# Kernel optimization log

Hardware: AMD Instinct MI355X
Metric: run time of the kernel (lower is better)

The kernel has to match this reference:

```python
import jax, jax.numpy as jnp
import numpy as np

B, S, E, H, L, D = 16, 512, 512, 8, 3, 64
OBS, ACT, NA = 128, 16, 8
KAPPAS = jnp.asarray(1.0 - 2.0 ** (-5.0 - np.arange(H)), jnp.float32)  # per-head retention decay, decay_scaling_factor=1.0
INV_SQRT_D = 1.0 / float(np.sqrt(D))


def rmsnorm(x, w, eps=1e-6):
    return x * jax.lax.rsqrt(jnp.mean(x * x, -1, keepdims=True) + eps) * w


def swiglu(x, wg, wp):
    return jax.nn.silu(x @ wg) * (x @ wp)


def sin_pe(ts, dim):
    # sinusoidal timestep positional encoding, ts: (B,S) float -> (B,S,dim)
    half = dim // 2
    freqs = jnp.exp(-np.log(10000.0) * jnp.arange(half, dtype=jnp.float32) / half)
    ang = ts[..., None] * freqs
    return jnp.concatenate([jnp.sin(ang), jnp.cos(ang)], -1)


def retention(xk, xq, xv, h0, ts, wq, wk, wv, wo, masked):
    # chunkwise multi-scale retention with cross-chunk recurrent state h0: (B,H,D,D)
    b, s, e = xq.shape
    pe = sin_pe(ts, e)
    q = ((xq + pe) @ wq).reshape(b, s, H, D).transpose(0, 2, 1, 3)            # (B,H,S,D)
    k = ((xk + pe) @ wk).reshape(b, s, H, D).transpose(0, 2, 1, 3) * INV_SQRT_D
    v = ((xv + pe) @ wv).reshape(b, s, H, D).transpose(0, 2, 1, 3)
    lk = jnp.log(KAPPAS)                                                      # (H,)
    diff = ts[:, None, :, None] - ts[:, None, None, :]                        # (B,1,S,S) timestep gaps
    if masked:
        idx = jnp.arange(s)
        allow = (diff > 0) | ((diff == 0) & (idx[:, None] >= idx[None, :]))
        dmat = jnp.where(allow, jnp.exp(lk[None, :, None, None] * diff), 0.0)
    else:
        dmat = jnp.exp(lk[None, :, None, None] * jnp.abs(diff))
    scores = jnp.einsum('bhnd,bhmd->bhnm', q, k) * dmat                       # decay-masked scores
    xi = jnp.exp(lk[None, :, None] * (ts[:, None, :] + 1.0))                  # (B,H,S) cross-chunk decay
    out = jnp.einsum('bhnm,bhmd->bhnd', scores, v) + jnp.einsum('bhnd,bhde->bhne', q, h0) * xi[..., None]
    tmax = ts.max(-1)                                                         # (B,)
    wst = jnp.exp(lk[None, :, None] * (tmax[:, None, None] - ts[:, None, :]))  # (B,H,S)
    h_new = jnp.exp(lk[None, :] * (tmax[:, None] + 1.0))[..., None, None] * h0 \
        + jnp.einsum('bhm,bhmd,bhme->bhde', wst, k, v)
    out = out.transpose(0, 2, 1, 3).reshape(b, s, e) @ wo
    return out, h_new


def _forward(obs, action, enc_hs, dec_hs1, dec_hs2, step_count, params):
    (eoln, eow, eln, ewq, ewk, ewv, ewo, eln1, eln2, efg, efp,
     ehw1, ehb1, ehln, ehw2, ehb2,
     daw, dln, dwq1, dwk1, dwv1, dwo1, dwq2, dwk2, dwv2, dwo2,
     dln1, dln2, dln3, dfg, dfp,
     dhw1, dhb1, dhln, dhw2, dhb2) = params
    ts = step_count.astype(jnp.float32)
    # ---- Encoder ----
    obs_rep = jax.nn.gelu(rmsnorm(obs, eoln) @ eow)
    enc_new = []
    for i in range(L):
        x = rmsnorm(obs_rep, eln)
        ret, hn = retention(x, x, x, enc_hs[:, i], ts, ewq[i], ewk[i], ewv[i], ewo[i], masked=False)
        x = rmsnorm(x + ret, eln1[i])
        obs_rep = rmsnorm(x + swiglu(x, efg[i], efp[i]), eln2[i])
        enc_new.append(hn)
    value = rmsnorm(jax.nn.gelu(obs_rep @ ehw1 + ehb1), ehln) @ ehw2 + ehb2
    # ---- Decoder ----
    x = rmsnorm(jax.nn.gelu(action @ daw), dln)
    d1_new, d2_new = [], []
    for i in range(L):
        ret, h1 = retention(x, x, x, dec_hs1[:, i], ts, dwq1[i], dwk1[i], dwv1[i], dwo1[i], masked=True)
        r = rmsnorm(x + ret, dln1[i])
        ret2, h2 = retention(r, obs_rep, r, dec_hs2[:, i], ts, dwq2[i], dwk2[i], dwv2[i], dwo2[i], masked=True)
        y = rmsnorm(obs_rep + ret2, dln2[i])
        x = rmsnorm(y + swiglu(y, dfg[i], dfp[i]), dln3[i])
        d1_new.append(h1)
        d2_new.append(h2)
    logits = rmsnorm(jax.nn.gelu(x @ dhw1 + dhb1), dhln) @ dhw2 + dhb2
    return value, logits, jnp.stack(enc_new, 1), jnp.stack(d1_new, 1), jnp.stack(d2_new, 1)


def setup_inputs():
    key = jax.random.key(0)
    ki = iter(jax.random.split(key, 50))
    def w(shape, s=0.02):
        return jax.random.normal(next(ki), shape, jnp.float32) * s
    inp = {
        'obs': jax.random.normal(next(ki), (B, S, OBS), jnp.float32),
        'action': jax.random.uniform(next(ki), (B, S, ACT + 1), jnp.float32),
        'enc_hs': jnp.zeros((B, L, H, D, D), jnp.float32),
        'dec_hs1': jnp.zeros((B, L, H, D, D), jnp.float32),
        'dec_hs2': jnp.zeros((B, L, H, D, D), jnp.float32),
        'step_count': jnp.broadcast_to(jnp.arange(S, dtype=jnp.int32) // NA, (B, S)),
        'enc_obs_ln_w': jnp.ones((OBS,), jnp.float32),
        'enc_obs_w': w((OBS, E)),
        'enc_ln_w': jnp.ones((E,), jnp.float32),
        'enc_wq': w((L, E, E)), 'enc_wk': w((L, E, E)), 'enc_wv': w((L, E, E)), 'enc_wo': w((L, E, E)),
        'enc_ln1_w': jnp.ones((L, E), jnp.float32), 'enc_ln2_w': jnp.ones((L, E), jnp.float32),
        'enc_ffn_gate': w((L, E, E)), 'enc_ffn_proj': w((L, E, E)),
        'enc_head_w1': w((E, E)), 'enc_head_b1': jnp.zeros((E,), jnp.float32),
        'enc_head_ln': jnp.ones((E,), jnp.float32),
        'enc_head_w2': w((E, 1)), 'enc_head_b2': jnp.zeros((1,), jnp.float32),
        'dec_act_w': w((ACT + 1, E)), 'dec_ln_w': jnp.ones((E,), jnp.float32),
        'dec_wq1': w((L, E, E)), 'dec_wk1': w((L, E, E)), 'dec_wv1': w((L, E, E)), 'dec_wo1': w((L, E, E)),
        'dec_wq2': w((L, E, E)), 'dec_wk2': w((L, E, E)), 'dec_wv2': w((L, E, E)), 'dec_wo2': w((L, E, E)),
        'dec_ln1_w': jnp.ones((L, E), jnp.float32), 'dec_ln2_w': jnp.ones((L, E), jnp.float32),
        'dec_ln3_w': jnp.ones((L, E), jnp.float32),
        'dec_ffn_gate': w((L, E, E)), 'dec_ffn_proj': w((L, E, E)),
        'dec_head_w1': w((E, E)), 'dec_head_b1': jnp.zeros((E,), jnp.float32),
        'dec_head_ln': jnp.ones((E,), jnp.float32),
        'dec_head_w2': w((E, ACT)), 'dec_head_b2': jnp.zeros((ACT,), jnp.float32),
    }
    return inp


def reference(obs, action, enc_hs, dec_hs1, dec_hs2, step_count, enc_obs_ln_w, enc_obs_w, enc_ln_w, enc_wq, enc_wk, enc_wv, enc_wo, enc_ln1_w, enc_ln2_w, enc_ffn_gate, enc_ffn_proj, enc_head_w1, enc_head_b1, enc_head_ln, enc_head_w2, enc_head_b2, dec_act_w, dec_ln_w, dec_wq1, dec_wk1, dec_wv1, dec_wo1, dec_wq2, dec_wk2, dec_wv2, dec_wo2, dec_ln1_w, dec_ln2_w, dec_ln3_w, dec_ffn_gate, dec_ffn_proj, dec_head_w1, dec_head_b1, dec_head_ln, dec_head_w2, dec_head_b2):
    params = (enc_obs_ln_w, enc_obs_w, enc_ln_w, enc_wq, enc_wk, enc_wv, enc_wo, enc_ln1_w, enc_ln2_w, enc_ffn_gate, enc_ffn_proj, enc_head_w1, enc_head_b1, enc_head_ln, enc_head_w2, enc_head_b2, dec_act_w, dec_ln_w, dec_wq1, dec_wk1, dec_wv1, dec_wo1, dec_wq2, dec_wk2, dec_wv2, dec_wo2, dec_ln1_w, dec_ln2_w, dec_ln3_w, dec_ffn_gate, dec_ffn_proj, dec_head_w1, dec_head_b1, dec_head_ln, dec_head_w2, dec_head_b2)
    return _forward(obs, action, enc_hs, dec_hs1, dec_hs2, step_count, params)
```

## Files before the change

kernel.cpp:

```cpp
#include <hip/hip_runtime.h>
#include <hip/hip_bf16.h>
#include <math.h>

typedef __attribute__((ext_vector_type(8))) short short8;
typedef __attribute__((ext_vector_type(4))) short short4v;
typedef __attribute__((ext_vector_type(4))) float f32x4;

#define BB 16
#define SS 512
#define EE 512
#define HH 8
#define DH 64
#define LL 3
#define MM (BB*SS)
#define OBSD 128
#define ACTD 17
#define INV_SQRT_D 0.125f

#define ACT_NONE 0
#define ACT_GELU 1

#define NORM_PLAIN 0
#define NORM_ADD 1

// ... 32 lines not shown
  for (int i = 0; i < 4; ++i){
    int k = gx*32 + ty + i*8, n = gy*32 + tx;
    t[ty+i*8][tx] = (k < K) ? src[(size_t)k*EE + n] : 0.f;
  }
  __syncthreads();
  #pragma unroll
  for (int i = 0; i < 4; ++i){
    int k = gx*32 + tx, n = gy*32 + ty + i*8;
    dst[(size_t)n*Kpad + k] = f2bs(t[tx][ty+i*8]);
  }
}

struct TP50 { const float* s[50]; unsigned short* d[50]; };
__global__ __launch_bounds__(256) void wtpose_batch_kernel(TP50 tp)
{
  __shared__ float t[32][33];
  const float* src = tp.s[blockIdx.z];
  unsigned short* dst = tp.d[blockIdx.z];
  const int gx = blockIdx.x, gy = blockIdx.y;
  const int tx = threadIdx.x, ty = threadIdx.y;
  #pragma unroll
  for (int i = 0; i < 4; ++i){
    int k = gx*32 + ty + i*8, n = gy*32 + tx;
    t[ty+i*8][tx] = src[(size_t)k*EE + n];
  }
  __syncthreads();
  #pragma unroll
  for (int i = 0; i < 4; ++i){
    int k = gx*32 + tx, n = gy*32 + ty + i*8;
    dst[(size_t)n*EE + k] = f2bs(t[tx][ty+i*8]);
  }
}

template<int MODE, int ENC>
__global__ __launch_bounds__(256) void gemm128_kernel(
    const unsigned short* __restrict__ A, const unsigned short* __restrict__ Wt,
    const float* __restrict__ bias, float* __restrict__ C,
    int Kpad, float scale, int act,
    int gstart, const int* __restrict__ tsi,
    unsigned short* __restrict__ qlo, unsigned short* __restrict__ qhi,
    unsigned short* __restrict__ klo, unsigned short* __restrict__ kloT,
    unsigned short* __restrict__ khi, unsigned short* __restrict__ khiT,
    unsigned short* __restrict__ vT)
{
  __shared__ unsigned short As[2][128*64];
  __shared__ unsigned short Bs[2][128*64];
  const int bm = blockIdx.y*128, bn = blockIdx.x*128;
  const int tid = threadIdx.x, lane = tid & 63, wv = tid >> 6;
  const int wr = wv >> 1, wc = wv & 1;
  const int l16 = lane & 15, quad = lane >> 4;

  f32x4 acc[4][4];
  #pragma unroll
  for (int i=0;i<4;i++)
    #pragma unroll
    for (int j=0;j<4;j++) acc[i][j]=(f32x4)(0.f);

  const int sg = lane >> 3;
  const int lg = (lane & 7) ^ sg;
  size_t aoff[4], boff[4];
  #pragma unroll
  for (int i=0;i<4;i++){
    aoff[i] = (size_t)(bm + wv*32 + i*8 + sg)*Kpad + lg*8;
    boff[i] = (size_t)(bn + wv*32 + i*8 + sg)*Kpad + lg*8;
  }
  const int swz = (l16 & 7) << 3;

  auto STAGE = [&](int buf, int t){
    const int k0 = t*64;
    #pragma unroll
    for (int i=0;i<4;i++){
      gl16(A + aoff[i] + k0, (char*)&As[buf][0] + ((wv*4+i) << 10));
      gl16(Wt + boff[i] + k0, (char*)&Bs[buf][0] + ((wv*4+i) << 10));
    }
  };
// ... 11 lines not shown
        bf[nt][ks] = *(const short8*)&Bs[buf][(wc*64 + nt*16 + l16)*64 + ((ks*32 + quad*8) ^ swz)];
    #pragma unroll
    for (int ks=0; ks<2; ++ks)
      #pragma unroll
      for (int mt=0; mt<4; ++mt)
        #pragma unroll
        for (int nt=0; nt<4; ++nt)
          acc[mt][nt] = __builtin_amdgcn_mfma_f32_16x16x32_bf16(af[mt][ks], bf[nt][ks], acc[mt][nt], 0, 0, 0);
  };

  const int NT = Kpad >> 6;
  STAGE(0, 0);
  PIPE_SYNC;
  int cur = 0;
  for (int t = 0; t < NT; ++t){
    if (t+1 < NT) STAGE(cur^1, t+1);
    COMPUTE(cur);
    if (t+1 < NT) PIPE_SYNC;
    cur ^= 1;
  }

  if (MODE == 0){
    #pragma unroll
    for (int mt=0; mt<4; ++mt){
      int rb = bm + wr*64 + mt*16 + quad*4;
      #pragma unroll
      for (int nt=0; nt<4; ++nt){
        int col = bn + wc*64 + nt*16 + l16;
        float bv = bias ? bias[col] : 0.f;
        #pragma unroll
        for (int j=0;j<4;j++){
          float v = acc[mt][nt][j]*scale + bv;
          if (act==ACT_GELU) v = gelu_f(v);
          C[(size_t)(rb+j)*EE + col] = v;
        }
      }
    }
  } else {
    const int group = gstart + (bn >> 9);
    const int hh = ((bn & 511) >> 6) + wc;
    const float lkh = lkappa(hh);
    const float scl = (group == 1) ? INV_SQRT_D : 1.f;
    const float dsg = (group == 1) ? -1.f : 1.f;
    #pragma unroll
    for (int mt=0; mt<4; ++mt){
      int rb = bm + wr*64 + mt*16 + quad*4;
      float e0[4], e1[4];
      if (group < 2){
        #pragma unroll
        for (int j=0;j<4;j++){
          float x = dsg*lkh*(float)tsi[rb+j];
          e0[j] = __expf(x); e1[j] = __expf(-x);
        }
      }
      int bloc = rb >> 9, m0 = rb & 511;
      #pragma unroll
      for (int nt=0; nt<4; ++nt){
        int ccol = (bn & 511) + wc*64 + nt*16 + l16;
        int ee = nt*16 + l16;
        size_t taddr = (((size_t)bloc*HH + hh)*DH + ee)*SS + m0;
        float vals[4];
        #pragma unroll
        for (int j=0;j<4;j++) vals[j] = acc[mt][nt][j]*scl;
        if (group == 0){
          #pragma unroll
          for (int j=0;j<4;j++) qlo[(size_t)(rb+j)*EE + ccol] = f2bs(vals[j]*e0[j]);
          if (ENC){
            #pragma unroll
            for (int j=0;j<4;j++) qhi[(size_t)(rb+j)*EE + ccol] = f2bs(vals[j]*e1[j]);
          }
        } else if (group == 1){
          short4v pk;
          #pragma unroll
          for (int j=0;j<4;j++){
            unsigned short v = f2bs(vals[j]*e0[j]);
            klo[(size_t)(rb+j)*EE + ccol] = v;
            pk[j] = (short)v;
          }
          *(short4v*)&kloT[taddr] = pk;
          if (ENC){
            short4v pk2;
            #pragma unroll
            for (int j=0;j<4;j++){
              unsigned short v = f2bs(vals[j]*e1[j]);
              khi[(size_t)(rb+j)*EE + ccol] = v;
              pk2[j] = (short)v;
            }
            *(short4v*)&khiT[taddr] = pk2;
          }
        } else {
          short4v pk;
          #pragma unroll
          for (int j=0;j<4;j++) pk[j] = (short)f2bs(vals[j]);
          *(short4v*)&vT[taddr] = pk;
        }
      }
    }
  }
}

__global__ __launch_bounds__(256) void gemm_sw_kernel(
    const unsigned short* __restrict__ A, const unsigned short* __restrict__ Wt,
    const unsigned short* __restrict__ Wt2, unsigned short* __restrict__ swo)
{
  __shared__ unsigned short As[2][128*64];
  __shared__ unsigned short Bs[2][64*64];
  __shared__ unsigned short Bs2[2][64*64];
  const int bm = blockIdx.y*128, bn = blockIdx.x*64;
  const int tid = threadIdx.x, lane = tid & 63, wv = tid >> 6;
  const int wr = wv >> 1, wc = wv & 1;
  const int l16 = lane & 15, quad = lane >> 4;

  f32x4 acc[4][2], acc2[4][2];
  #pragma unroll
  for (int i=0;i<4;i++){
    acc[i][0]=(f32x4)(0.f); acc[i][1]=(f32x4)(0.f);
    acc2[i][0]=(f32x4)(0.f); acc2[i][1]=(f32x4)(0.f);
  }

  const int sg = lane >> 3;
  const int lg = (lane & 7) ^ sg;
  size_t aoff[4], boff[2];
  #pragma unroll
  for (int i=0;i<4;i++)
    aoff[i] = (size_t)(bm + (wv*4+i)*8 + sg)*EE + lg*8;
  #pragma unroll
// ... 32 lines not shown
      #pragma unroll
      for (int mt=0; mt<4; ++mt)
        #pragma unroll
        for (int nt=0; nt<2; ++nt){
          acc[mt][nt]  = __builtin_amdgcn_mfma_f32_16x16x32_bf16(af[mt][ks], bf[nt][ks],  acc[mt][nt],  0, 0, 0);
          acc2[mt][nt] = __builtin_amdgcn_mfma_f32_16x16x32_bf16(af[mt][ks], bf2[nt][ks], acc2[mt][nt], 0, 0, 0);
        }
  };

  STAGE(0, 0);
  PIPE_SYNC;
  int cur = 0;
  for (int t = 0; t < 8; ++t){
    if (t+1 < 8) STAGE(cur^1, t+1);
    COMPUTE(cur);
    if (t+1 < 8) PIPE_SYNC;
    cur ^= 1;
  }

  #pragma unroll
  for (int mt=0; mt<4; ++mt){
    int rb = bm + wr*64 + mt*16 + quad*4;
    #pragma unroll
    for (int nt=0; nt<2; ++nt){
      int col = bn + wc*32 + nt*16 + l16;
      #pragma unroll
      for (int j=0;j<4;j++)
        swo[(size_t)(rb+j)*EE + col] = f2bs(silu_f(acc[mt][nt][j])*acc2[mt][nt][j]);
    }
  }
}

__global__ __launch_bounds__(256) void norm_b_kernel(
    const float* __restrict__ af, const unsigned short* __restrict__ ab,
    const float* __restrict__ res, const unsigned short* __restrict__ resb,
    const float* __restrict__ w, unsigned short* __restrict__ o1,
    unsigned short* __restrict__ o2, const unsigned short* __restrict__ peb,
    int mode)
{
  const int row = blockIdx.x*4 + (threadIdx.x >> 6);
  const int lane = threadIdx.x & 63;
  const size_t base = (size_t)row*EE + lane*8;
  float t[8];
  if (ab){
    short8 av = *(const short8*)&ab[base];
    #pragma unroll
    for (int e=0;e<8;++e) t[e] = bs2f((unsigned short)av[e]);
  } else {
    float4 a0 = *(const float4*)&af[base];
    float4 a1 = *(const float4*)&af[base+4];
    t[0]=a0.x;t[1]=a0.y;t[2]=a0.z;t[3]=a0.w;t[4]=a1.x;t[5]=a1.y;t[6]=a1.z;t[7]=a1.w;
  }
  if (mode == NORM_ADD){
    if (resb){
      short8 rv = *(const short8*)&resb[base];
      #pragma unroll
      for (int e=0;e<8;++e) t[e] += bs2f((unsigned short)rv[e]);
    } else {
      float4 r0 = *(const float4*)&res[base];
      float4 r1 = *(const float4*)&res[base+4];
      t[0]+=r0.x;t[1]+=r0.y;t[2]+=r0.z;t[3]+=r0.w;t[4]+=r1.x;t[5]+=r1.y;t[6]+=r1.z;t[7]+=r1.w;
    }
  }
  float ss = 0.f;
  #pragma unroll
  for (int e=0;e<8;++e) ss += t[e]*t[e];
  #pragma unroll
  for (int o=32;o;o>>=1) ss += __shfl_xor(ss, o);
  float r = 1.f/sqrtf(ss/(float)EE + 1e-6f);
  float4 w0 = *(const float4*)&w[lane*8];
  float4 w1 = *(const float4*)&w[lane*8+4];
  float y[8];
  y[0]=t[0]*r*w0.x; y[1]=t[1]*r*w0.y; y[2]=t[2]*r*w0.z; y[3]=t[3]*r*w0.w;
  y[4]=t[4]*r*w1.x; y[5]=t[5]*r*w1.y; y[6]=t[6]*r*w1.z; y[7]=t[7]*r*w1.w;
  short8 pk;
  #pragma unroll
  for (int e=0;e<8;++e) pk[e] = (short)f2bs(y[e]);
  *(short8*)&o1[base] = pk;
  if (o2){
    short8 pv = *(const short8*)&peb[base];
    short8 pz;
    #pragma unroll
    for (int e=0;e<8;++e) pz[e] = (short)f2bs(y[e] + bs2f((unsigned short)pv[e]));
    *(short8*)&o2[base] = pz;
  }
}

__global__ __launch_bounds__(256) void norm_obs_kernel(
    const float* __restrict__ a, const float* __restrict__ w, unsigned short* __restrict__ o)
{
  const int row = blockIdx.x*4 + (threadIdx.x >> 6);
  const int lane = threadIdx.x & 63;
  const size_t base = (size_t)row*OBSD + lane*2;
  float2 av = *(const float2*)&a[base];
  float ss = av.x*av.x + av.y*av.y;
  #pragma unroll
  for (int off=32;off;off>>=1) ss += __shfl_xor(ss, off);
  float r = 1.f/sqrtf(ss/(float)OBSD + 1e-6f);
  float2 wv2 = *(const float2*)&w[lane*2];
  unsigned int pk = (unsigned int)f2bs(av.x*r*wv2.x) | ((unsigned int)f2bs(av.y*r*wv2.y) << 16);
  *(unsigned int*)&o[base] = pk;
}

__global__ __launch_bounds__(256) void act_embed_kernel(
    const float* __restrict__ a, unsigned short* __restrict__ o)
{
  int idx = blockIdx.x*256 + threadIdx.x;
  int row = idx >> 6, col = idx & 63;
  o[idx] = (col < ACTD) ? f2bs(a[(size_t)row*ACTD + col]) : 0;
}

__global__ __launch_bounds__(256) void wchunkscan_kernel(
    const unsigned short* __restrict__ kloT, const unsigned short* __restrict__ khiT,
    const unsigned short* __restrict__ vT,
    const float* __restrict__ h0, const float* __restrict__ tmx,
    unsigned short* __restrict__ wcum_lo, unsigned short* __restrict__ wcum_hi,
    float* __restrict__ hnew, int enc)
{
  __shared__ unsigned short vsh[64*72];
  __shared__ unsigned short ksh[64*72];
  const int h = blockIdx.x, b = blockIdx.y;
  const int tid = threadIdx.x, lane = tid & 63, wv = tid >> 6;
  const int quad = lane >> 4, l16 = lane & 15;
  const float lk = lkappa(h);
  const float elk = __expf(lk);
  const float etm = __expf(lk*tmx[b]);
  const size_t wbase = ((size_t)b*HH + h)*8*4096;
  const size_t hbase = (size_t)b*(LL*HH*DH*DH) + (size_t)h*(DH*DH);
  const int e0r = wv*16 + quad*4;
  const int sr = tid >> 2, sseg = (tid & 3)*16;

  f32x4 cum[4];
  #pragma unroll
  for (int dt=0; dt<4; ++dt)
    #pragma unroll
    for (int j=0;j<4;j++)
      cum[dt][j] = elk * h0[hbase + (size_t)(dt*16+l16)*64 + e0r + j];

  for (int c = 0; c < 8; ++c){
    __syncthreads();
    {
      const unsigned short* vrow = vT   + (((size_t)b*HH + h)*DH + sr)*SS + c*64 + sseg;
      const unsigned short* krow = kloT + (((size_t)b*HH + h)*DH + sr)*SS + c*64 + sseg;
      #pragma unroll
      for (int i = 0; i < 2; ++i){
        *(short8*)&vsh[sr*72 + sseg + i*8] = *(const short8*)(vrow + i*8);
        *(short8*)&ksh[sr*72 + sseg + i*8] = *(const short8*)(krow + i*8);
      }
    }
    __syncthreads();
    short8 av[2];
    #pragma unroll
    for (int ks=0; ks<2; ++ks)
      av[ks] = *(const short8*)&vsh[(wv*16 + l16)*72 + ks*32 + quad*8];
    f32x4 acc[4];
    #pragma unroll
    for (int dt=0; dt<4; ++dt) acc[dt] = (f32x4)(0.f);
    #pragma unroll
    for (int ks=0; ks<2; ++ks)
      #pragma unroll
      for (int dt=0; dt<4; ++dt){
        short8 kb = *(const short8*)&ksh[(dt*16 + l16)*72 + ks*32 + quad*8];
        acc[dt] = __builtin_amdgcn_mfma_f32_16x16x32_bf16(av[ks], kb, acc[dt], 0, 0, 0);
      }
    #pragma unroll
    for (int dt=0; dt<4; ++dt)
      #pragma unroll
      for (int j=0;j<4;j++){
        wcum_lo[wbase + (size_t)c*4096 + (size_t)(e0r+j)*64 + dt*16 + l16] = f2bs(cum[dt][j]);
        cum[dt][j] += acc[dt][j];
      }
  }
  #pragma unroll
  for (int dt=0; dt<4; ++dt)
    #pragma unroll
    for (int j=0;j<4;j++)
      hnew[hbase + (size_t)(dt*16+l16)*64 + e0r + j] = etm * cum[dt][j];

  if (enc){
    f32x4 suf[4];
    #pragma unroll
    for (int dt=0; dt<4; ++dt) suf[dt] = (f32x4)(0.f);
    for (int c = 7; c >= 0; --c){
      __syncthreads();
      {
        const unsigned short* vrow = vT   + (((size_t)b*HH + h)*DH + sr)*SS + c*64 + sseg;
        const unsigned short* krow = khiT + (((size_t)b*HH + h)*DH + sr)*SS + c*64 + sseg;
        #pragma unroll
        for (int i = 0; i < 2; ++i){
          *(short8*)&vsh[sr*72 + sseg + i*8] = *(const short8*)(vrow + i*8);
          *(short8*)&ksh[sr*72 + sseg + i*8] = *(const short8*)(krow + i*8);
        }
      }
      __syncthreads();
      short8 av[2];
      #pragma unroll
      for (int ks=0; ks<2; ++ks)
        av[ks] = *(const short8*)&vsh[(wv*16 + l16)*72 + ks*32 + quad*8];
      f32x4 acc[4];
      #pragma unroll
      for (int dt=0; dt<4; ++dt) acc[dt] = (f32x4)(0.f);
      #pragma unroll
      for (int ks=0; ks<2; ++ks)
        #pragma unroll
        for (int dt=0; dt<4; ++dt){
          short8 kb = *(const short8*)&ksh[(dt*16 + l16)*72 + ks*32 + quad*8];
          acc[dt] = __builtin_amdgcn_mfma_f32_16x16x32_bf16(av[ks], kb, acc[dt], 0, 0, 0);
        }
      #pragma unroll
      for (int dt=0; dt<4; ++dt)
        #pragma unroll
        for (int j=0;j<4;j++){
          wcum_hi[wbase + (size_t)c*4096 + (size_t)(e0r+j)*64 + dt*16 + l16] = f2bs(suf[dt][j]);
          suf[dt][j] += acc[dt][j];
        }
    }
  }
}

template<int ENC>
__global__ __launch_bounds__(256) void retention2_kernel(
    const unsigned short* __restrict__ qlo, const unsigned short* __restrict__ qhi,
    const unsigned short* __restrict__ klo, const unsigned short* __restrict__ khi,
    const unsigned short* __restrict__ vT,
    const unsigned short* __restrict__ wlo, const unsigned short* __restrict__ whi,
    const int* __restrict__ tsi, unsigned short* __restrict__ outp)
{
  __shared__ unsigned short qsh[64*72];
  __shared__ unsigned short wsh[64*72];
  __shared__ unsigned short ksh[64*72];
  __shared__ unsigned short vsh[64*72];
  __shared__ unsigned short qsh2[ENC ? 64*72 : 2];
  __shared__ unsigned short wsh2[ENC ? 64*72 : 2];
  __shared__ float tsf[SS];
  const int b = blockIdx.z, h = blockIdx.y, t = blockIdx.x;
  const int n0 = t*64;
  const int tid = threadIdx.x, lane = tid & 63, wv = tid >> 6;
  const int quad = lane >> 4, l16 = lane & 15;

  for (int i = tid; i < SS; i += 256) tsf[i] = (float)tsi[b*SS + i];
  {
    const int n = tid >> 2, seg = (tid & 3)*16;
    const unsigned short* qr = qlo + ((size_t)b*SS + n0 + n)*EE + h*DH + seg;
    #pragma unroll
    for (int i = 0; i < 2; ++i)
      *(short8*)&qsh[n*72 + seg + i*8] = *(const short8*)(qr + i*8);
    const unsigned short* wr = wlo + (((size_t)b*HH + h)*8 + t)*4096 + (size_t)n*64 + seg;
    #pragma unroll
    for (int i = 0; i < 2; ++i)
      *(short8*)&wsh[n*72 + seg + i*8] = *(const short8*)(wr + i*8);
    if (ENC){
      const unsigned short* qr2 = qhi + ((size_t)b*SS + n0 + n)*EE + h*DH + seg;
      #pragma unroll
      for (int i = 0; i < 2; ++i)
        *(short8*)&qsh2[n*72 + seg + i*8] = *(const short8*)(qr2 + i*8);
      const unsigned short* wr2 = whi + (((size_t)b*HH + h)*8 + t)*4096 + (size_t)n*64 + seg;
      #pragma unroll
      for (int i = 0; i < 2; ++i)
        *(short8*)&wsh2[n*72 + seg + i*8] = *(const short8*)(wr2 + i*8);
    }
  }
  __syncthreads();

  const int rowbase = wv*16;
  short8 qa[2], qa2[2];
  #pragma unroll
  for (int ks=0; ks<2; ++ks)
    qa[ks] = *(const short8*)&qsh[(rowbase + l16)*72 + ks*32 + quad*8];
  if (ENC){
    #pragma unroll
    for (int ks=0; ks<2; ++ks)
      qa2[ks] = *(const short8*)&qsh2[(rowbase + l16)*72 + ks*32 + quad*8];
  }

  float tn = tsf[n0 + lane];
  float maxn = tn, minn = tn;
  #pragma unroll
  for (int o=32;o;o>>=1){
    maxn = fmaxf(maxn, __shfl_xor(maxn, o));
    minn = fminf(minn, __shfl_xor(minn, o));
  }

  f32x4 acc_o[4];
  #pragma unroll
  for (int et=0; et<4; ++et){
    f32x4 a = (f32x4)(0.f);
    #pragma unroll
    for (int ks=0; ks<2; ++ks){
      short8 wb = *(const short8*)&wsh[(et*16 + l16)*72 + ks*32 + quad*8];
      a = __builtin_amdgcn_mfma_f32_16x16x32_bf16(qa[ks], wb, a, 0, 0, 0);
    }
    if (ENC){
      #pragma unroll
      for (int ks=0; ks<2; ++ks){
        short8 wb2 = *(const short8*)&wsh2[(et*16 + l16)*72 + ks*32 + quad*8];
        a = __builtin_amdgcn_mfma_f32_16x16x32_bf16(qa2[ks], wb2, a, 0, 0, 0);
      }
    }
    acc_o[et] = a;
  }

  for (int c = 0; c < 8; ++c){
    const int mc = c*64;
    float tmv = tsf[mc + lane];
    float maxm = tmv, minm = tmv;
    #pragma unroll
    for (int o=32;o;o>>=1){
      maxm = fmaxf(maxm, __shfl_xor(maxm, o));
      minm = fminf(minm, __shfl_xor(minm, o));
    }
    if (ENC){
      if (maxm <= minn) continue;
      if (minm >= maxn) continue;
    } else {
      if ((maxm < minn) || (maxm == minn && (mc + 63) < n0)) continue;
      if (minm > maxn) continue;
    }
    __syncthreads();
    {
      const int m = tid >> 2, cb = (tid & 3)*16;
      const unsigned short* krow = klo + ((size_t)b*SS + mc + m)*EE + h*DH + cb;
      #pragma unroll
      for (int i = 0; i < 2; ++i)
        *(short8*)&ksh[m*72 + cb + i*8] = *(const short8*)(krow + i*8);
      const unsigned short* vrow = vT + (((size_t)b*HH + h)*DH + m)*SS + mc + cb;
      #pragma unroll
      for (int i = 0; i < 2; ++i)
        *(short8*)&vsh[m*72 + cb + i*8] = *(const short8*)(vrow + i*8);
      if (ENC){
        const unsigned short* k2row = khi + ((size_t)b*SS + mc + m)*EE + h*DH + cb;
        #pragma unroll
        for (int i = 0; i < 2; ++i)
          *(short8*)&qsh2[m*72 + cb + i*8] = *(const short8*)(k2row + i*8);
      }
    }
    __syncthreads();
    f32x4 sacc[4], sacc2[4];
    #pragma unroll
    for (int mt=0; mt<4; ++mt){
      f32x4 a = (f32x4)(0.f);
      #pragma unroll
      for (int ks=0; ks<2; ++ks){
        short8 kb = *(const short8*)&ksh[(mt*16 + l16)*72 + ks*32 + quad*8];
        a = __builtin_amdgcn_mfma_f32_16x16x32_bf16(qa[ks], kb, a, 0, 0, 0);
      }
      sacc[mt] = a;
      if (ENC){
        f32x4 a2 = (f32x4)(0.f);
        #pragma unroll
        for (int ks=0; ks<2; ++ks){
          short8 kb2 = *(const short8*)&qsh2[(mt*16 + l16)*72 + ks*32 + quad*8];
          a2 = __builtin_amdgcn_mfma_f32_16x16x32_bf16(qa2[ks], kb2, a2, 0, 0, 0);
        }
        sacc2[mt] = a2;
      }
    }
    float tsm[4]; int mg[4];
    #pragma unroll
    for (int mt=0; mt<4; ++mt){ mg[mt] = mc + mt*16 + l16; tsm[mt] = tsf[mg[mt]]; }
    #pragma unroll
    for (int j=0;j<4;j++){
      int nloc = rowbase + quad*4 + j;
      int n = n0 + nloc;
      float tsn = tsf[n];
      #pragma unroll
      for (int mt=0; mt<4; ++mt){
        float diff = tsn - tsm[mt];
// ... 120 lines not shown
  const float* ehw1 = (const float*)d_in[17];
  const float* ehb1 = (const float*)d_in[18];
  const float* ehln = (const float*)d_in[19];
  const float* ehw2 = (const float*)d_in[20];
  const float* ehb2 = (const float*)d_in[21];
  const float* daw  = (const float*)d_in[22];
  const float* dln  = (const float*)d_in[23];
  const float* dwq1 = (const float*)d_in[24];
  const float* dwk1 = (const float*)d_in[25];
  const float* dwv1 = (const float*)d_in[26];
  const float* dwo1 = (const float*)d_in[27];
  const float* dwq2 = (const float*)d_in[28];
  const float* dwk2 = (const float*)d_in[29];
  const float* dwv2 = (const float*)d_in[30];
  const float* dwo2 = (const float*)d_in[31];
  const float* dln1 = (const float*)d_in[32];
  const float* dln2 = (const float*)d_in[33];
  const float* dln3 = (const float*)d_in[34];
  const float* dfg  = (const float*)d_in[35];
  const float* dfp  = (const float*)d_in[36];
  const float* dhw1 = (const float*)d_in[37];
  const float* dhb1 = (const float*)d_in[38];
  const float* dhln = (const float*)d_in[39];
  const float* dhw2 = (const float*)d_in[40];
  const float* dhb2 = (const float*)d_in[41];

  const size_t BUF = (size_t)MM*EE;
  float* wsf  = (float*)d_ws;
  float* f32a = wsf;
  float* f32b = f32a + BUF;
  float* tmx  = f32b + BUF;
  unsigned short* wcum_lo = (unsigned short*)f32a;
  unsigned short* wcum_hi = wcum_lo + BUF;
  unsigned short* sw_b    = (unsigned short*)f32b;
  unsigned short* ub = (unsigned short*)(tmx + 64);
  unsigned short* xrep_b    = ub;  ub += BUF;
  unsigned short* xrep_pe_b = ub;  ub += BUF;
  unsigned short* x_b       = ub;  ub += BUF;
  unsigned short* x_pe_b    = ub;  ub += BUF;
  unsigned short* t1_b      = ub;  ub += BUF;
  unsigned short* t1_pe_b   = ub;  ub += BUF;
  unsigned short* peb       = ub;  ub += BUF;
  unsigned short* qlo_b     = ub;  ub += BUF;
  unsigned short* klo_b     = ub;  ub += BUF;
  unsigned short* kloT_b    = ub;  ub += BUF;
  unsigned short* khi_b     = ub;  ub += BUF;
  unsigned short* khiT_b    = ub;  ub += BUF;
  unsigned short* vT_b      = ub;  ub += BUF;
  unsigned short* obs_n     = ub;  ub += (size_t)MM*OBSD;
  unsigned short* act_b     = obs_n;
  unsigned short* qhi_b     = t1_pe_b;
  const size_t W55 = (size_t)EE*EE;
  unsigned short* wts = ub;  ub += 50*W55;
  unsigned short* wt_eow = ub; ub += (size_t)EE*OBSD;
  unsigned short* wt_daw = ub; ub += (size_t)EE*64;
  size_t need = (char*)ub - (char*)d_ws;
  if (ws_size < need) return;

  unsigned short* wt_eqkv  = wts + 0*W55;
  unsigned short* wt_ewo   = wts + 9*W55;
  unsigned short* wt_efg   = wts + 12*W55;
  unsigned short* wt_efp   = wts + 15*W55;
  unsigned short* wt_ehw1  = wts + 18*W55;
  unsigned short* wt_dqkv1 = wts + 19*W55;
  unsigned short* wt_dwo1  = wts + 28*W55;
  unsigned short* wt_dkv2  = wts + 31*W55;
  unsigned short* wt_dwq2  = wts + 37*W55;
  unsigned short* wt_dwo2  = wts + 40*W55;
  unsigned short* wt_dfg   = wts + 43*W55;
  unsigned short* wt_dfp   = wts + 46*W55;
  unsigned short* wt_dhw1  = wts + 49*W55;

  float* out        = (float*)d_out;
  float* value_out  = out;
  float* logits_out = out + 8192;
  float* enc_out    = logits_out + (size_t)MM*16;
  float* d1_out     = enc_out + (size_t)BB*LL*HH*DH*DH;
  float* d2_out     = d1_out  + (size_t)BB*LL*HH*DH*DH;

  const size_t HS_L = (size_t)HH*DH*DH;

  {
    TP50 tp;
    int z = 0;
    auto add = [&](const float* p){ tp.s[z] = p; tp.d[z] = wts + (size_t)z*W55; ++z; };
    for (int i=0;i<3;++i){ add(ewq+i*W55); add(ewk+i*W55); add(ewv+i*W55); }
    for (int i=0;i<3;++i) add(ewo+i*W55);
    for (int i=0;i<3;++i) add(efg+i*W55);
    for (int i=0;i<3;++i) add(efp+i*W55);
    add(ehw1);
    for (int i=0;i<3;++i){ add(dwq1+i*W55); add(dwk1+i*W55); add(dwv1+i*W55); }
    for (int i=0;i<3;++i) add(dwo1+i*W55);
    for (int i=0;i<3;++i){ add(dwk2+i*W55); add(dwv2+i*W55); }
    for (int i=0;i<3;++i) add(dwq2+i*W55);
    for (int i=0;i<3;++i) add(dwo2+i*W55);
    for (int i=0;i<3;++i) add(dfg+i*W55);
    for (int i=0;i<3;++i) add(dfp+i*W55);
    add(dhw1);
    wtpose_batch_kernel<<<dim3(16,16,50), dim3(32,8), 0, stream>>>(tp);
  }
  wtpose_kernel<<<dim3(4,16), dim3(32,8), 0, stream>>>(eow, wt_eow, OBSD, OBSD);
  wtpose_kernel<<<dim3(2,16), dim3(32,8), 0, stream>>>(daw, wt_daw, ACTD, 64);

  pe_kernel<<<(MM*EE)/256, 256, 0, stream>>>(stepc, peb);
  tsmax_kernel<<<BB, 256, 0, stream>>>(stepc, tmx);

  auto gemmF = [&](const unsigned short* A, const unsigned short* Wt, const float* bias,
                   float* C, int Kpad, float scale, int act){
    gemm128_kernel<0,0><<<dim3(EE/128, MM/128), 256, 0, stream>>>(A, Wt, bias, C,
        Kpad, scale, act, 0, nullptr,
        nullptr, nullptr, nullptr, nullptr, nullptr, nullptr, nullptr);
  };
  auto gemmQKV = [&](const unsigned short* A, const unsigned short* Wt, int enc){
    if (enc)
      gemm128_kernel<1,1><<<dim3(12, MM/128), 256, 0, stream>>>(A, Wt, nullptr, nullptr,
          EE, 1.f, ACT_NONE, 0, stepc,
          qlo_b, qhi_b, klo_b, kloT_b, khi_b, khiT_b, vT_b);
    else
      gemm128_kernel<1,0><<<dim3(12, MM/128), 256, 0, stream>>>(A, Wt, nullptr, nullptr,
          EE, 1.f, ACT_NONE, 0, stepc,
          qlo_b, nullptr, klo_b, kloT_b, nullptr, nullptr, vT_b);
  };
  auto gemmKV = [&](const unsigned short* A, const unsigned short* Wt){
    gemm128_kernel<1,0><<<dim3(8, MM/128), 256, 0, stream>>>(A, Wt, nullptr, nullptr,
        EE, 1.f, ACT_NONE, 1, stepc,
        nullptr, nullptr, klo_b, kloT_b, nullptr, nullptr, vT_b);
  };
  auto gemmQ2 = [&](const unsigned short* A, const unsigned short* Wt){
    gemm128_kernel<1,0><<<dim3(4, MM/128), 256, 0, stream>>>(A, Wt, nullptr, nullptr,
        EE, 1.f, ACT_NONE, 0, stepc,
        qlo_b, nullptr, nullptr, nullptr, nullptr, nullptr, nullptr);
  };
  auto gemmSW = [&](const unsigned short* A, const unsigned short* Wg, const unsigned short* Wp){
    gemm_sw_kernel<<<dim3(EE/64, MM/128), 256, 0, stream>>>(A, Wg, Wp, sw_b);
  };
  auto norm = [&](const float* af, const unsigned short* ab, const float* res,
                  const unsigned short* resb, const float* w,
                  unsigned short* o1, unsigned short* o2, int mode){
    norm_b_kernel<<<MM/4, 256, 0, stream>>>(af, ab, res, resb, w, o1, o2, peb, mode);
  };
  auto retention = [&](const float* h0, float* hnew, unsigned short* o, int enc){
    wchunkscan_kernel<<<dim3(HH, BB), 256, 0, stream>>>(kloT_b, khiT_b, vT_b,
        h0, tmx, wcum_lo, enc ? wcum_hi : wcum_lo, hnew, enc);
    if (enc)
      retention2_kernel<1><<<dim3(8, HH, BB), 256, 0, stream>>>(
          qlo_b, qhi_b, klo_b, khi_b, vT_b, wcum_lo, wcum_hi, stepc, o);
    else
      retention2_kernel<0><<<dim3(8, HH, BB), 256, 0, stream>>>(
          qlo_b, nullptr, klo_b, nullptr, vT_b, wcum_lo, nullptr, stepc, o);
  };

  norm_obs_kernel<<<MM/4, 256, 0, stream>>>(obs, eoln, obs_n);
  gemmF(obs_n, wt_eow, nullptr, f32a, OBSD, 1.f, ACT_GELU);

  for (int i = 0; i < LL; ++i){
    if (i == 0) norm(f32a, nullptr, nullptr, nullptr, eln, x_b, x_pe_b, NORM_PLAIN);
    else        norm(nullptr, xrep_b, nullptr, nullptr, eln, x_b, x_pe_b, NORM_PLAIN);
    gemmQKV(x_pe_b, wt_eqkv + (size_t)3*i*W55, 1);
    retention(enc_hs + i*HS_L, enc_out + i*HS_L, t1_b, 1);
    gemmF(t1_b, wt_ewo + i*W55, nullptr, f32a, EE, 1.f, ACT_NONE);
    norm(nullptr, x_b, f32a, nullptr, eln1 + i*EE, t1_b, nullptr, NORM_ADD);
    gemmSW(t1_b, wt_efg + i*W55, wt_efp + i*W55);
    norm(nullptr, t1_b, nullptr, sw_b, eln2 + i*EE, xrep_b, xrep_pe_b, NORM_ADD);
  }

  gemmF(xrep_b, wt_ehw1, ehb1, f32a, EE, 1.f, ACT_GELU);
  norm(f32a, nullptr, nullptr, nullptr, ehln, t1_b, nullptr, NORM_PLAIN);
  value_head_kernel<<<MM/32, 256, 0, stream>>>(t1_b, ehw2, ehb2, value_out);

  act_embed_kernel<<<(MM*64)/256, 256, 0, stream>>>(action, act_b);
  gemmF(act_b, wt_daw, nullptr, f32a, 64, 1.f, ACT_GELU);
  norm(f32a, nullptr, nullptr, nullptr, dln, x_b, x_pe_b, NORM_PLAIN);

  for (int i = 0; i < LL; ++i){
    gemmQKV(x_pe_b, wt_dqkv1 + (size_t)3*i*W55, 0);
    retention(dec_hs1 + i*HS_L, d1_out + i*HS_L, t1_b, 0);
    gemmF(t1_b, wt_dwo1 + i*W55, nullptr, f32a, EE, 1.f, ACT_NONE);
    norm(nullptr, x_b, f32a, nullptr, dln1 + i*EE, t1_b, t1_pe_b, NORM_ADD);
    gemmQ2(xrep_pe_b, wt_dwq2 + i*W55);
    gemmKV(t1_pe_b, wt_dkv2 + (size_t)2*i*W55);
    retention(dec_hs2 + i*HS_L, d2_out + i*HS_L, t1_b, 0);
    gemmF(t1_b, wt_dwo2 + i*W55, nullptr, f32a, EE, 1.f, ACT_NONE);
    norm(nullptr, xrep_b, f32a, nullptr, dln2 + i*EE, x_b, nullptr, NORM_ADD);
    gemmSW(x_b, wt_dfg + i*W55, wt_dfp + i*W55);
    norm(nullptr, x_b, nullptr, sw_b, dln3 + i*EE, x_b, x_pe_b, NORM_ADD);
  }

  gemmF(x_b, wt_dhw1, dhb1, f32a, EE, 1.f, ACT_GELU);
  norm(f32a, nullptr, nullptr, nullptr, dhln, t1_b, nullptr, NORM_PLAIN);
  logits_head_kernel<<<MM/16, 256, 0, stream>>>(t1_b, dhw2, dhb2, logits_out);
}
```

Measured before the change: 1.247 ms.

## Store plain bf16 Q/K and apply timestep decay inside retention kernels

```diff
diff --git a/kernel.cpp b/kernel.cpp
--- a/kernel.cpp
+++ b/kernel.cpp
@@ -88,15 +88,12 @@
   }
 }
 
-template<int MODE, int ENC>
+template<int MODE>
 __global__ __launch_bounds__(256) void gemm128_kernel(
     const unsigned short* __restrict__ A, const unsigned short* __restrict__ Wt,
-    const float* __restrict__ bias, float* __restrict__ C,
-    int Kpad, float scale, int act,
-    int gstart, const int* __restrict__ tsi,
-    unsigned short* __restrict__ qlo, unsigned short* __restrict__ qhi,
-    unsigned short* __restrict__ klo, unsigned short* __restrict__ kloT,
-    unsigned short* __restrict__ khi, unsigned short* __restrict__ khiT,
+    const float* __restrict__ bias, unsigned short* __restrict__ Cb,
+    int Kpad, float scale, int act, int gstart,
+    unsigned short* __restrict__ qout, unsigned short* __restrict__ kout,
     unsigned short* __restrict__ vT)
 {
   __shared__ unsigned short As[2][128*64];
@@ -174,66 +171,39 @@
         for (int j=0;j<4;j++){
           float v = acc[mt][nt][j]*scale + bv;
           if (act==ACT_GELU) v = gelu_f(v);
-          C[(size_t)(rb+j)*EE + col] = v;
+          Cb[(size_t)(rb+j)*EE + col] = f2bs(v);
         }
       }
     }
   } else {
     const int group = gstart + (bn >> 9);
-    const int hh = ((bn & 511) >> 6) + wc;
-    const float lkh = lkappa(hh);
-    const float scl = (group == 1) ? INV_SQRT_D : 1.f;
-    const float dsg = (group == 1) ? -1.f : 1.f;
-    #pragma unroll
-    for (int mt=0; mt<4; ++mt){
-      int rb = bm + wr*64 + mt*16 + quad*4;
-      float e0[4], e1[4];
-      if (group < 2){
-        #pragma unroll
-        for (int j=0;j<4;j++){
-          float x = dsg*lkh*(float)tsi[rb+j];
-          e0[j] = __expf(x); e1[j] = __expf(-x);
+    if (group <= 1){
+      unsigned short* O = (group == 0) ? qout : kout;
+      const float scl = (group == 1) ? INV_SQRT_D : 1.f;
+      #pragma unroll
+      for (int mt=0; mt<4; ++mt){
+        int rb = bm + wr*64 + mt*16 + quad*4;
+        #pragma unroll
+        for (int nt=0; nt<4; ++nt){
+          int ccol = (bn & 511) + wc*64 + nt*16 + l16;
+          #pragma unroll
+          for (int j=0;j<4;j++)
+            O[(size_t)(rb+j)*EE + ccol] = f2bs(acc[mt][nt][j]*scl);
         }
       }
-      int bloc = rb >> 9, m0 = rb & 511;
-      #pragma unroll
-      for (int nt=0; nt<4; ++nt){
-        int ccol = (bn & 511) + wc*64 + nt*16 + l16;
-        int ee = nt*16 + l16;
-        size_t taddr = (((size_t)bloc*HH + hh)*DH + ee)*SS + m0;
-        float vals[4];
-        #pragma unroll
-        for (int j=0;j<4;j++) vals[j] = acc[mt][nt][j]*scl;
-        if (group == 0){
-          #pragma unroll
-          for (int j=0;j<4;j++) qlo[(size_t)(rb+j)*EE + ccol] = f2bs(vals[j]*e0[j]);
-          if (ENC){
-            #pragma unroll
-            for (int j=0;j<4;j++) qhi[(size_t)(rb+j)*EE + ccol] = f2bs(vals[j]*e1[j]);
-          }
-        } else if (group == 1){
+    } else {
+      const int hh = ((bn & 511) >> 6) + wc;
+      #pragma unroll
+      for (int mt=0; mt<4; ++mt){
+        int rb = bm + wr*64 + mt*16 + quad*4;
+        int bloc = rb >> 9, m0 = rb & 511;
+        #pragma unroll
+        for (int nt=0; nt<4; ++nt){
+          int ee = nt*16 + l16;
+          size_t taddr = (((size_t)bloc*HH + hh)*DH + ee)*SS + m0;
           short4v pk;
           #pragma unroll
-          for (int j=0;j<4;j++){
-            unsigned short v = f2bs(vals[j]*e0[j]);
-            klo[(size_t)(rb+j)*EE + ccol] = v;
-            pk[j] = (short)v;
-          }
-          *(short4v*)&kloT[taddr] = pk;
-          if (ENC){
-            short4v pk2;
-            #pragma unroll
-            for (int j=0;j<4;j++){
-              unsigned short v = f2bs(vals[j]*e1[j]);
-              khi[(size_t)(rb+j)*EE + ccol] = v;
-              pk2[j] = (short)v;
-            }
-            *(short4v*)&khiT[taddr] = pk2;
-          }
-        } else {
-          short4v pk;
-          #pragma unroll
-          for (int j=0;j<4;j++) pk[j] = (short)f2bs(vals[j]);
+          for (int j=0;j<4;j++) pk[j] = (short)f2bs(acc[mt][nt][j]);
           *(short4v*)&vT[taddr] = pk;
         }
       }
@@ -332,8 +302,7 @@
 }
 
 __global__ __launch_bounds__(256) void norm_b_kernel(
-    const float* __restrict__ af, const unsigned short* __restrict__ ab,
-    const float* __restrict__ res, const unsigned short* __restrict__ resb,
+    const unsigned short* __restrict__ ab, const unsigned short* __restrict__ resb,
     const float* __restrict__ w, unsigned short* __restrict__ o1,
     unsigned short* __restrict__ o2, const unsigned short* __restrict__ peb,
     int mode)
@@ -342,25 +311,15 @@
   const int lane = threadIdx.x & 63;
   const size_t base = (size_t)row*EE + lane*8;
   float t[8];
-  if (ab){
+  {
     short8 av = *(const short8*)&ab[base];
     #pragma unroll
     for (int e=0;e<8;++e) t[e] = bs2f((unsigned short)av[e]);
-  } else {
-    float4 a0 = *(const float4*)&af[base];
-    float4 a1 = *(const float4*)&af[base+4];
-    t[0]=a0.x;t[1]=a0.y;t[2]=a0.z;t[3]=a0.w;t[4]=a1.x;t[5]=a1.y;t[6]=a1.z;t[7]=a1.w;
   }
   if (mode == NORM_ADD){
-    if (resb){
-      short8 rv = *(const short8*)&resb[base];
-      #pragma unroll
-      for (int e=0;e<8;++e) t[e] += bs2f((unsigned short)rv[e]);
-    } else {
-      float4 r0 = *(const float4*)&res[base];
-      float4 r1 = *(const float4*)&res[base+4];
-      t[0]+=r0.x;t[1]+=r0.y;t[2]+=r0.z;t[3]+=r0.w;t[4]+=r1.x;t[5]+=r1.y;t[6]+=r1.z;t[7]+=r1.w;
-    }
+    short8 rv = *(const short8*)&resb[base];
+    #pragma unroll
+    for (int e=0;e<8;++e) t[e] += bs2f((unsigned short)rv[e]);
   }
   float ss = 0.f;
   #pragma unroll
@@ -411,9 +370,9 @@
 }
 
 __global__ __launch_bounds__(256) void wchunkscan_kernel(
-    const unsigned short* __restrict__ kloT, const unsigned short* __restrict__ khiT,
-    const unsigned short* __restrict__ vT,
+    const unsigned short* __restrict__ k, const unsigned short* __restrict__ vT,
     const float* __restrict__ h0, const float* __restrict__ tmx,
+    const int* __restrict__ tsi,
     unsigned short* __restrict__ wcum_lo, unsigned short* __restrict__ wcum_hi,
     float* __restrict__ hnew, int enc)
 {
@@ -440,12 +399,18 @@
   for (int c = 0; c < 8; ++c){
     __syncthreads();
     {
-      const unsigned short* vrow = vT   + (((size_t)b*HH + h)*DH + sr)*SS + c*64 + sseg;
-      const unsigned short* krow = kloT + (((size_t)b*HH + h)*DH + sr)*SS + c*64 + sseg;
+      const unsigned short* vrow = vT + (((size_t)b*HH + h)*DH + sr)*SS + c*64 + sseg;
+      #pragma unroll
+      for (int i = 0; i < 2; ++i)
+        *(short8*)&vsh[sr*72 + sseg + i*8] = *(const short8*)(vrow + i*8);
+      float els = __expf(-lk * (float)tsi[b*SS + c*64 + sr]);
+      const unsigned short* krow = k + ((size_t)b*SS + c*64 + sr)*EE + h*DH + sseg;
       #pragma unroll
       for (int i = 0; i < 2; ++i){
-        *(short8*)&vsh[sr*72 + sseg + i*8] = *(const short8*)(vrow + i*8);
-        *(short8*)&ksh[sr*72 + sseg + i*8] = *(const short8*)(krow + i*8);
+        short8 kv = *(const short8*)(krow + i*8);
+        #pragma unroll
+        for (int e = 0; e < 8; ++e)
+          ksh[(sseg + i*8 + e)*72 + sr] = f2bs(bs2f((unsigned short)kv[e])*els);
       }
     }
     __syncthreads();
@@ -484,12 +449,18 @@
     for (int c = 7; c >= 0; --c){
       __syncthreads();
       {
-        const unsigned short* vrow = vT   + (((size_t)b*HH + h)*DH + sr)*SS + c*64 + sseg;
-        const unsigned short* krow = khiT + (((size_t)b*HH + h)*DH + sr)*SS + c*64 + sseg;
+        const unsigned short* vrow = vT + (((size_t)b*HH + h)*DH + sr)*SS + c*64 + sseg;
+        #pragma unroll
+        for (int i = 0; i < 2; ++i)
+          *(short8*)&vsh[sr*72 + sseg + i*8] = *(const short8*)(vrow + i*8);
+        float ehs = __expf(lk * (float)tsi[b*SS + c*64 + sr]);
+        const unsigned short* krow = k + ((size_t)b*SS + c*64 + sr)*EE + h*DH + sseg;
         #pragma unroll
         for (int i = 0; i < 2; ++i){
-          *(short8*)&vsh[sr*72 + sseg + i*8] = *(const short8*)(vrow + i*8);
-          *(short8*)&ksh[sr*72 + sseg + i*8] = *(const short8*)(krow + i*8);
+          short8 kv = *(const short8*)(krow + i*8);
+          #pragma unroll
+          for (int e = 0; e < 8; ++e)
+            ksh[(sseg + i*8 + e)*72 + sr] = f2bs(bs2f((unsigned short)kv[e])*ehs);
         }
       }
       __syncthreads();
@@ -520,8 +491,7 @@
 
 template<int ENC>
 __global__ __launch_bounds__(256) void retention2_kernel(
-    const unsigned short* __restrict__ qlo, const unsigned short* __restrict__ qhi,
-    const unsigned short* __restrict__ klo, const unsigned short* __restrict__ khi,
+    const unsigned short* __restrict__ q, const unsigned short* __restrict__ k,
     const unsigned short* __restrict__ vT,
     const unsigned short* __restrict__ wlo, const unsigned short* __restrict__ whi,
     const int* __restrict__ tsi, unsigned short* __restrict__ outp)
@@ -537,23 +507,33 @@
   const int n0 = t*64;
   const int tid = threadIdx.x, lane = tid & 63, wv = tid >> 6;
   const int quad = lane >> 4, l16 = lane & 15;
+  const float lk = lkappa(h);
 
   for (int i = tid; i < SS; i += 256) tsf[i] = (float)tsi[b*SS + i];
   {
     const int n = tid >> 2, seg = (tid & 3)*16;
-    const unsigned short* qr = qlo + ((size_t)b*SS + n0 + n)*EE + h*DH + seg;
-    #pragma unroll
-    for (int i = 0; i < 2; ++i)
-      *(short8*)&qsh[n*72 + seg + i*8] = *(const short8*)(qr + i*8);
+    float ts_n = (float)tsi[b*SS + n0 + n];
+    float e0 = __expf(lk*ts_n);
+    float e1 = ENC ? __expf(-lk*ts_n) : 0.f;
+    const unsigned short* qr = q + ((size_t)b*SS + n0 + n)*EE + h*DH + seg;
+    #pragma unroll
+    for (int i = 0; i < 2; ++i){
+      short8 v = *(const short8*)(qr + i*8);
+      short8 o, o2;
+      #pragma unroll
+      for (int e=0;e<8;++e){
+        float f = bs2f((unsigned short)v[e]);
+        o[e] = (short)f2bs(f*e0);
+        if (ENC) o2[e] = (short)f2bs(f*e1);
+      }
+      *(short8*)&qsh[n*72 + seg + i*8] = o;
+      if (ENC) *(short8*)&qsh2[n*72 + seg + i*8] = o2;
+    }
     const unsigned short* wr = wlo + (((size_t)b*HH + h)*8 + t)*4096 + (size_t)n*64 + seg;
     #pragma unroll
     for (int i = 0; i < 2; ++i)
       *(short8*)&wsh[n*72 + seg + i*8] = *(const short8*)(wr + i*8);
     if (ENC){
-      const unsigned short* qr2 = qhi + ((size_t)b*SS + n0 + n)*EE + h*DH + seg;
-      #pragma unroll
-      for (int i = 0; i < 2; ++i)
-        *(short8*)&qsh2[n*72 + seg + i*8] = *(const short8*)(qr2 + i*8);
       const unsigned short* wr2 = whi + (((size_t)b*HH + h)*8 + t)*4096 + (size_t)n*64 + seg;
       #pragma unroll
       for (int i = 0; i < 2; ++i)
@@ -619,20 +599,27 @@
     __syncthreads();
     {
       const int m = tid >> 2, cb = (tid & 3)*16;
-      const unsigned short* krow = klo + ((size_t)b*SS + mc + m)*EE + h*DH + cb;
-      #pragma unroll
-      for (int i = 0; i < 2; ++i)
-        *(short8*)&ksh[m*72 + cb + i*8] = *(const short8*)(krow + i*8);
+      float ts_m = tsf[mc + m];
+      float ek0 = __expf(-lk*ts_m);
+      float ek1 = ENC ? __expf(lk*ts_m) : 0.f;
+      const unsigned short* krow = k + ((size_t)b*SS + mc + m)*EE + h*DH + cb;
+      #pragma unroll
+      for (int i = 0; i < 2; ++i){
+        short8 kv = *(const short8*)(krow + i*8);
+        short8 o, o2;
+        #pragma unroll
+        for (int e=0;e<8;++e){
+          float f = bs2f((unsigned short)kv[e]);
+          o[e] = (short)f2bs(f*ek0);
+          if (ENC) o2[e] = (short)f2bs(f*ek1);
+        }
+        *(short8*)&ksh[m*72 + cb + i*8] = o;
+        if (ENC) *(short8*)&qsh2[m*72 + cb + i*8] = o2;
+      }
       const unsigned short* vrow = vT + (((size_t)b*HH + h)*DH + m)*SS + mc + cb;
       #pragma unroll
       for (int i = 0; i < 2; ++i)
         *(short8*)&vsh[m*72 + cb + i*8] = *(const short8*)(vrow + i*8);
-      if (ENC){
-        const unsigned short* k2row = khi + ((size_t)b*SS + mc + m)*EE + h*DH + cb;
-        #pragma unroll
-        for (int i = 0; i < 2; ++i)
-          *(short8*)&qsh2[m*72 + cb + i*8] = *(const short8*)(k2row + i*8);
-      }
     }
     __syncthreads();
     f32x4 sacc[4], sacc2[4];
@@ -819,6 +806,7 @@
   float* tmx  = f32b + BUF;
   unsigned short* wcum_lo = (unsigned short*)f32a;
   unsigned short* wcum_hi = wcum_lo + BUF;
+  unsigned short* gf_b    = wcum_lo;
   unsigned short* sw_b    = (unsigned short*)f32b;
   unsigned short* ub = (unsigned short*)(tmx + 64);
   unsigned short* xrep_b    = ub;  ub += BUF;
@@ -828,15 +816,11 @@
   unsigned short* t1_b      = ub;  ub += BUF;
   unsigned short* t1_pe_b   = ub;  ub += BUF;
   unsigned short* peb       = ub;  ub += BUF;
-  unsigned short* qlo_b     = ub;  ub += BUF;
-  unsigned short* klo_b     = ub;  ub += BUF;
-  unsigned short* kloT_b    = ub;  ub += BUF;
-  unsigned short* khi_b     = ub;  ub += BUF;
-  unsigned short* khiT_b    = ub;  ub += BUF;
+  unsigned short* q_b       = ub;  ub += BUF;
+  unsigned short* k_b       = ub;  ub += BUF;
   unsigned short* vT_b      = ub;  ub += BUF;
   unsigned short* obs_n     = ub;  ub += (size_t)MM*OBSD;
   unsigned short* act_b     = obs_n;
-  unsigned short* qhi_b     = t1_pe_b;
   const size_t W55 = (size_t)EE*EE;
   unsigned short* wts = ub;  ub += 50*W55;
   unsigned short* wt_eow = ub; ub += (size_t)EE*OBSD;
@@ -893,87 +877,77 @@
   tsmax_kernel<<<BB, 256, 0, stream>>>(stepc, tmx);
 
   auto gemmF = [&](const unsigned short* A, const unsigned short* Wt, const float* bias,
-                   float* C, int Kpad, float scale, int act){
-    gemm128_kernel<0,0><<<dim3(EE/128, MM/128), 256, 0, stream>>>(A, Wt, bias, C,
-        Kpad, scale, act, 0, nullptr,
-        nullptr, nullptr, nullptr, nullptr, nullptr, nullptr, nullptr);
-  };
-  auto gemmQKV = [&](const unsigned short* A, const unsigned short* Wt, int enc){
-    if (enc)
-      gemm128_kernel<1,1><<<dim3(12, MM/128), 256, 0, stream>>>(A, Wt, nullptr, nullptr,
-          EE, 1.f, ACT_NONE, 0, stepc,
-          qlo_b, qhi_b, klo_b, kloT_b, khi_b, khiT_b, vT_b);
-    else
-      gemm128_kernel<1,0><<<dim3(12, MM/128), 256, 0, stream>>>(A, Wt, nullptr, nullptr,
-          EE, 1.f, ACT_NONE, 0, stepc,
-          qlo_b, nullptr, klo_b, kloT_b, nullptr, nullptr, vT_b);
+                   unsigned short* Cb, int Kpad, float scale, int act){
+    gemm128_kernel<0><<<dim3(EE/128, MM/128), 256, 0, stream>>>(A, Wt, bias, Cb,
+        Kpad, scale, act, 0, nullptr, nullptr, nullptr);
+  };
+  auto gemmQKV = [&](const unsigned short* A, const unsigned short* Wt){
+    gemm128_kernel<1><<<dim3(12, MM/128), 256, 0, stream>>>(A, Wt, nullptr, nullptr,
+        EE, 1.f, ACT_NONE, 0, q_b, k_b, vT_b);
   };
   auto gemmKV = [&](const unsigned short* A, const unsigned short* Wt){
-    gemm128_kernel<1,0><<<dim3(8, MM/128), 256, 0, stream>>>(A, Wt, nullptr, nullptr,
-        EE, 1.f, ACT_NONE, 1, stepc,
-        nullptr, nullptr, klo_b, kloT_b, nullptr, nullptr, vT_b);
+    gemm128_kernel<1><<<dim3(8, MM/128), 256, 0, stream>>>(A, Wt, nullptr, nullptr,
+        EE, 1.f, ACT_NONE, 1, nullptr, k_b, vT_b);
   };
   auto gemmQ2 = [&](const unsigned short* A, const unsigned short* Wt){
-    gemm128_kernel<1,0><<<dim3(4, MM/128), 256, 0, stream>>>(A, Wt, nullptr, nullptr,
-        EE, 1.f, ACT_NONE, 0, stepc,
-        qlo_b, nullptr, nullptr, nullptr, nullptr, nullptr, nullptr);
+    gemm128_kernel<1><<<dim3(4, MM/128), 256, 0, stream>>>(A, Wt, nullptr, nullptr,
+        EE, 1.f, ACT_NONE, 0, q_b, nullptr, nullptr);
   };
   auto gemmSW = [&](const unsigned short* A, const unsigned short* Wg, const unsigned short* Wp){
     gemm_sw_kernel<<<dim3(EE/64, MM/128), 256, 0, stream>>>(A, Wg, Wp, sw_b);
   };
-  auto norm = [&](const float* af, const unsigned short* ab, const float* res,
-                  const unsigned short* resb, const float* w,
+  auto norm = [&](const unsigned short* ab, const unsigned short* resb, const float* w,
                   unsigned short* o1, unsigned short* o2, int mode){
-    norm_b_kernel<<<MM/4, 256, 0, stream>>>(af, ab, res, resb, w, o1, o2, peb, mode);
+    norm_b_kernel<<<MM/4, 256, 0, stream>>>(ab, resb, w, o1, o2, peb, mode);
   };
   auto retention = [&](const float* h0, float* hnew, unsigned short* o, int enc){
-    wchunkscan_kernel<<<dim3(HH, BB), 256, 0, stream>>>(kloT_b, khiT_b, vT_b,
-        h0, tmx, wcum_lo, enc ? wcum_hi : wcum_lo, hnew, enc);
+    wchunkscan_kernel<<<dim3(HH, BB), 256, 0, stream>>>(k_b, vT_b,
+        h0, tmx, stepc, wcum_lo, enc ? wcum_hi : wcum_lo, hnew, enc);
     if (enc)
       retention2_kernel<1><<<dim3(8, HH, BB), 256, 0, stream>>>(
-          qlo_b, qhi_b, klo_b, khi_b, vT_b, wcum_lo, wcum_hi, stepc, o);
+          q_b, k_b, vT_b, wcum_lo, wcum_hi, stepc, o);
     else
       retention2_kernel<0><<<dim3(8, HH, BB), 256, 0, stream>>>(
-          qlo_b, nullptr, klo_b, nullptr, vT_b, wcum_lo, nullptr, stepc, o);
+          q_b, k_b, vT_b, wcum_lo, nullptr, stepc, o);
   };
 
   norm_obs_kernel<<<MM/4, 256, 0, stream>>>(obs, eoln, obs_n);
-  gemmF(obs_n, wt_eow, nullptr, f32a, OBSD, 1.f, ACT_GELU);
+  gemmF(obs_n, wt_eow, nullptr, gf_b, OBSD, 1.f, ACT_GELU);
 
   for (int i = 0; i < LL; ++i){
-    if (i == 0) norm(f32a, nullptr, nullptr, nullptr, eln, x_b, x_pe_b, NORM_PLAIN);
-    else        norm(nullptr, xrep_b, nullptr, nullptr, eln, x_b, x_pe_b, NORM_PLAIN);
-    gemmQKV(x_pe_b, wt_eqkv + (size_t)3*i*W55, 1);
+    if (i == 0) norm(gf_b, nullptr, eln, x_b, x_pe_b, NORM_PLAIN);
+    else        norm(xrep_b, nullptr, eln, x_b, x_pe_b, NORM_PLAIN);
+    gemmQKV(x_pe_b, wt_eqkv + (size_t)3*i*W55);
     retention(enc_hs + i*HS_L, enc_out + i*HS_L, t1_b, 1);
-    gemmF(t1_b, wt_ewo + i*W55, nullptr, f32a, EE, 1.f, ACT_NONE);
-    norm(nullptr, x_b, f32a, nullptr, eln1 + i*EE, t1_b, nullptr, NORM_ADD);
+    gemmF(t1_b, wt_ewo + i*W55, nullptr, gf_b, EE, 1.f, ACT_NONE);
+    norm(x_b, gf_b, eln1 + i*EE, t1_b, nullptr, NORM_ADD);
     gemmSW(t1_b, wt_efg + i*W55, wt_efp + i*W55);
-    norm(nullptr, t1_b, nullptr, sw_b, eln2 + i*EE, xrep_b, xrep_pe_b, NORM_ADD);
-  }
-
-  gemmF(xrep_b, wt_ehw1, ehb1, f32a, EE, 1.f, ACT_GELU);
-  norm(f32a, nullptr, nullptr, nullptr, ehln, t1_b, nullptr, NORM_PLAIN);
+    norm(t1_b, sw_b, eln2 + i*EE, xrep_b, xrep_pe_b, NORM_ADD);
+  }
+
+  gemmF(xrep_b, wt_ehw1, ehb1, gf_b, EE, 1.f, ACT_GELU);
+  norm(gf_b, nullptr, ehln, t1_b, nullptr, NORM_PLAIN);
   value_head_kernel<<<MM/32, 256, 0, stream>>>(t1_b, ehw2, ehb2, value_out);
 
   act_embed_kernel<<<(MM*64)/256, 256, 0, stream>>>(action, act_b);
-  gemmF(act_b, wt_daw, nullptr, f32a, 64, 1.f, ACT_GELU);
-  norm(f32a, nullptr, nullptr, nullptr, dln, x_b, x_pe_b, NORM_PLAIN);
+  gemmF(act_b, wt_daw, nullptr, gf_b, 64, 1.f, ACT_GELU);
+  norm(gf_b, nullptr, dln, x_b, x_pe_b, NORM_PLAIN);
 
   for (int i = 0; i < LL; ++i){
-    gemmQKV(x_pe_b, wt_dqkv1 + (size_t)3*i*W55, 0);
+    gemmQKV(x_pe_b, wt_dqkv1 + (size_t)3*i*W55);
     retention(dec_hs1 + i*HS_L, d1_out + i*HS_L, t1_b, 0);
-    gemmF(t1_b, wt_dwo1 + i*W55, nullptr, f32a, EE, 1.f, ACT_NONE);
-    norm(nullptr, x_b, f32a, nullptr, dln1 + i*EE, t1_b, t1_pe_b, NORM_ADD);
+    gemmF(t1_b, wt_dwo1 + i*W55, nullptr, gf_b, EE, 1.f, ACT_NONE);
+    norm(x_b, gf_b, dln1 + i*EE, t1_b, t1_pe_b, NORM_ADD);
     gemmQ2(xrep_pe_b, wt_dwq2 + i*W55);
     gemmKV(t1_pe_b, wt_dkv2 + (size_t)2*i*W55);
     retention(dec_hs2 + i*HS_L, d2_out + i*HS_L, t1_b, 0);
-    gemmF(t1_b, wt_dwo2 + i*W55, nullptr, f32a, EE, 1.f, ACT_NONE);
-    norm(nullptr, xrep_b, f32a, nullptr, dln2 + i*EE, x_b, nullptr, NORM_ADD);
+    gemmF(t1_b, wt_dwo2 + i*W55, nullptr, gf_b, EE, 1.f, ACT_NONE);
+    norm(xrep_b, gf_b, dln2 + i*EE, x_b, nullptr, NORM_ADD);
     gemmSW(x_b, wt_dfg + i*W55, wt_dfp + i*W55);
-    norm(nullptr, x_b, nullptr, sw_b, dln3 + i*EE, x_b, x_pe_b, NORM_ADD);
-  }
-
-  gemmF(x_b, wt_dhw1, dhb1, f32a, EE, 1.f, ACT_GELU);
-  norm(f32a, nullptr, nullptr, nullptr, dhln, t1_b, nullptr, NORM_PLAIN);
+    norm(x_b, sw_b, dln3 + i*EE, x_b, x_pe_b, NORM_ADD);
+  }
+
+  gemmF(x_b, wt_dhw1, dhb1, gf_b, EE, 1.f, ACT_GELU);
+  norm(gf_b, nullptr, dhln, t1_b, nullptr, NORM_PLAIN);
   logits_head_kernel<<<MM/16, 256, 0, stream>>>(t1_b, dhw2, dhb2, logits_out);
 }
```

New measurement: 1.169 ms. 1.07x faster.
